# Performance work log

Hardware: AMD Instinct MI355X
Metric: run time of the kernel (lower is better)

## Reference

```python
import jax, jax.numpy as jnp
import numpy as np

NUM_HEADS = 8
NUM_LEVELS = 4
NUM_POINTS = 4


def setup_inputs() -> dict:
    key = jax.random.key(0)
    kq, kp, kv, k1, k2, k3, k4 = jax.random.split(key, 7)
    B, Q, C = 4, 4096, 256
    M, L, P = NUM_HEADS, NUM_LEVELS, NUM_POINTS
    shapes_np = np.array([[128, 128], [64, 64], [32, 32], [16, 16]], dtype=np.int32)
    sizes = shapes_np[:, 0] * shapes_np[:, 1]
    N = int(sizes.sum())  # 21760
    level_index = jnp.asarray(np.concatenate([[0], np.cumsum(sizes)[:-1]]).astype(np.int32))
    q = jax.random.normal(kq, (B, Q, C), jnp.float32)
    p = jax.random.uniform(kp, (B, Q, L, 2), jnp.float32)  # normalized ref points
    v = jax.random.normal(kv, (B, N, C), jnp.float32)
    # proj_offset bias: radial grid init from reset_parameters()
    t = np.arange(M, dtype=np.float32) * (2.0 * np.pi / M)
    grid = np.stack([np.cos(t), np.sin(t)], -1)
    grid = grid / np.abs(grid).max(-1, keepdims=True)
    grid = np.tile(grid[:, None, None, :], (1, L, P, 1)) * np.arange(1, P + 1, dtype=np.float32)[None, None, :, None]
    b_off = jnp.asarray(grid.reshape(-1))
    s = 1.0 / np.sqrt(C).astype(np.float32)
    W_off = jax.random.normal(k1, (C, M * L * P * 2), jnp.float32) * 0.01
    W_attn = jax.random.normal(k2, (C, M * L * P), jnp.float32) * s
    b_attn = jnp.zeros((M * L * P,), jnp.float32)
    W_val = jax.random.normal(k3, (C, C), jnp.float32) * s
    b_val = jnp.zeros((C,), jnp.float32)
    W_out = jax.random.normal(k4, (C, C), jnp.float32) * s
    b_out = jnp.zeros((C,), jnp.float32)
    return {"q": q, "p": p, "v": v, "shapes": jnp.asarray(shapes_np), "level_index": level_index,
            "W_off": W_off, "b_off": b_off, "W_attn": W_attn, "b_attn": b_attn,
            "W_val": W_val, "b_val": b_val, "W_out": W_out, "b_out": b_out}


def _ms_deform_attn(q, p, v, shapes, level_index, W_off, b_off, W_attn, b_attn, W_val, b_val, W_out, b_out):
    B, Q, C = q.shape
    M, L, P = NUM_HEADS, NUM_LEVELS, NUM_POINTS
    D = C // M
    N = v.shape[1]
    # value projection -> [B, M, N, D] (head-major for gather)
    v_p = (v @ W_val + b_val).reshape(B, N, M, D).transpose(0, 2, 1, 3)
    # attention weights, softmax over L*P (classic MSDeformAttn kernel contract)
    attn = jax.nn.softmax((q @ W_attn + b_attn).reshape(B, Q, M, L * P), axis=-1)
    attn = attn.reshape(B, Q, M, L, P)
    # sampling locations (P==2 reference-point branch)
    off = (q @ W_off + b_off).reshape(B, Q, M, L, P, 2)
    norm = jnp.stack([shapes[:, 1], shapes[:, 0]], -1).astype(jnp.float32)  # (W, H) per level
    loc = p[:, :, None, :, None, :] + off / norm[None, None, None, :, None, :]  # [B,Q,M,L,P,2]

    out = jnp.zeros((B, M, Q, D), jnp.float32)
    for l in range(L):
        Hf = shapes[l, 0].astype(jnp.float32)
        Wf = shapes[l, 1].astype(jnp.float32)
        Hi = shapes[l, 0]
        Wi = shapes[l, 1]
        base = level_index[l]
        # grid_sample(align_corners=False) convention: pixel = loc*size - 0.5
        x = loc[:, :, :, l, :, 0] * Wf - 0.5  # [B,Q,M,P]
        y = loc[:, :, :, l, :, 1] * Hf - 0.5
        x0 = jnp.floor(x)
        y0 = jnp.floor(y)
        lx, ly = x - x0, y - y0
        x0i = x0.astype(jnp.int32)
        y0i = y0.astype(jnp.int32)

        def corner(xi, yi, w):
            valid = (xi >= 0) & (xi < Wi) & (yi >= 0) & (yi < Hi)
            idx = base + jnp.clip(yi, 0, Hi - 1) * Wi + jnp.clip(xi, 0, Wi - 1)  # [B,Q,M,P]
            idx = idx.transpose(0, 2, 1, 3).reshape(B, M, Q * P)
            g = jnp.take_along_axis(v_p, idx[..., None], axis=2).reshape(B, M, Q, P, D)
            wv = (w * valid.astype(w.dtype)).transpose(0, 2, 1, 3)[..., None]  # [B,M,Q,P,1]
            return g * wv

        samp = (corner(x0i, y0i, (1 - lx) * (1 - ly))
                + corner(x0i + 1, y0i, lx * (1 - ly))
                + corner(x0i, y0i + 1, (1 - lx) * ly)
                + corner(x0i + 1, y0i + 1, lx * ly))  # [B,M,Q,P,D]
        a_l = attn[:, :, :, l, :].transpose(0, 2, 1, 3)  # [B,M,Q,P]
        out = out + jnp.einsum('bmqpd,bmqp->bmqd', samp, a_l)

    out = out.transpose(0, 2, 1, 3).reshape(B, Q, M * D)
    return out @ W_out + b_out


def reference(q, p, v, shapes, level_index, W_off, b_off, W_attn, b_attn, W_val, b_val, W_out, b_out):
    return _ms_deform_attn(q, p, v, shapes, level_index, W_off, b_off, W_attn, b_attn, W_val, b_val, W_out, b_out)
```

## Files before the change

kernel.cpp:

```cpp
#include <hip/hip_runtime.h>
#include <cstddef>

#define BB 4
#define QQ 4096
#define MM 8
#define NN 21760

typedef __bf16 bf16_8 __attribute__((ext_vector_type(8)));
typedef __bf16 bf16_4 __attribute__((ext_vector_type(4)));
typedef float  floatx4 __attribute__((ext_vector_type(4)));

__global__ __launch_bounds__(256) void prep_weights(
    const float* __restrict__ Wv, const float* __restrict__ Wa,
    const float* __restrict__ Wo, const float* __restrict__ Wu,
    const float* __restrict__ ba, const float* __restrict__ bo,
    __bf16* __restrict__ Wt, float* __restrict__ biasq)
{
    const int gid = blockIdx.x * 256 + threadIdx.x;
    if (gid < 65536) {
        const int n = gid >> 8, k = gid & 255;
        Wt[gid] = (__bf16)Wv[k * 256 + n];
    } else if (gid < 163840) {
        const int o = gid - 65536;
        const int n = o >> 8, k = o & 255;
        Wt[gid] = (__bf16)(n < 128 ? Wa[k * 128 + n] : Wo[k * 256 + (n - 128)]);
    } else if (gid < 229376) {
        const int o = gid - 163840;
        const int n = o >> 8, k = o & 255;
        Wt[gid] = (__bf16)Wu[k * 256 + n];
    } else if (gid < 229760) {
        const int j = gid - 229376;
        biasq[j] = (j < 128) ? ba[j] : bo[j - 128];
    }
}

__global__ __launch_bounds__(512, 4) void gemm_vq(
    const float* __restrict__ v,
    const float* __restrict__ q,
    const __bf16* __restrict__ Wt,
    const float* __restrict__ b_val,
    const float* __restrict__ biasq,
    __bf16* __restrict__ vpb,
    float* __restrict__ gqp)
{
    __shared__ __bf16 As[64][256];

    const int tid  = threadIdx.x;
    const int lane = tid & 63;
    const int wave = tid >> 6;
    const int quad = lane >> 4;
    const int l16  = lane & 15;
    const int flat = blockIdx.x;

    if (flat >= 768) {
        const int f2     = flat - 768;
        const int z      = f2 / 340;
        const int token0 = (f2 - z * 340) * 64;
        const float* Af  = v + (size_t)z * NN * 256;

        #pragma unroll
        for (int c = 0; c < 8; ++c) {
            const int cid = c * 512 + tid;
            const int r   = cid >> 6;
            const int kc  = (cid & 63) * 4;
            const float4 av = *(const float4*)(Af + (size_t)(token0 + r) * 256 + kc);
            bf16_4 w;
            w[0] = (__bf16)av.x; w[1] = (__bf16)av.y;
            w[2] = (__bf16)av.z; w[3] = (__bf16)av.w;
            const int col = ((((kc >> 3) ^ (r & 7)) << 3) | (kc & 7));
            *(bf16_4*)&As[r][col] = w;
        }

        bf16_8 wf[8][2];
        #pragma unroll
        for (int kk = 0; kk < 8; ++kk)
            #pragma unroll
            for (int j = 0; j < 2; ++j)
                wf[kk][j] = *(const bf16_8*)(Wt + (size_t)(wave * 32 + j * 16 + l16) * 256
                                              + kk * 32 + quad * 8);
        __syncthreads();

        floatx4 acc[2][4] = {};
        #pragma unroll
        for (int kk = 0; kk < 8; ++kk) {
            bf16_8 af[4];
            #pragma unroll
            for (int it = 0; it < 4; ++it)
                af[it] = *(const bf16_8*)&As[it * 16 + l16]
                                           [(((kk * 4 + quad) ^ (l16 & 7)) << 3)];
            #pragma unroll
            for (int j = 0; j < 2; ++j)
                #pragma unroll
                for (int it = 0; it < 4; ++it)
                    acc[j][it] = __builtin_amdgcn_mfma_f32_16x16x32_bf16(wf[kk][j], af[it], acc[j][it], 0, 0, 0);
        }

        #pragma unroll
        for (int j = 0; j < 2; ++j) {
            const int n0 = wave * 32 + j * 16 + quad * 4;
            const float4 b4 = *(const float4*)(b_val + n0);
            const int mh = n0 >> 5, dd = n0 & 31;
            #pragma unroll
            for (int it = 0; it < 4; ++it) {
                const int token = token0 + it * 16 + l16;
                bf16_4 ob;
                ob[0] = (__bf16)(acc[j][it][0] + b4.x);
                ob[1] = (__bf16)(acc[j][it][1] + b4.y);
                ob[2] = (__bf16)(acc[j][it][2] + b4.z);
                ob[3] = (__bf16)(acc[j][it][3] + b4.w);
                *(bf16_4*)(vpb + (((size_t)z * 8 + mh) * NN + token) * 32 + dd) = ob;
            }
        }
    } else {
        const int o      = flat;
        const int slice  = o >> 8;
        const int token0 = (o & 255) * 64;
        const int col0   = slice * 128;
        const __bf16* Wb = Wt + 65536 + (size_t)col0 * 256;

        #pragma unroll
        for (int c = 0; c < 8; ++c) {
            const int cid = c * 512 + tid;
            const int r   = cid >> 6;
            const int kc  = (cid & 63) * 4;
            const float4 av = *(const float4*)(q + (size_t)(token0 + r) * 256 + kc);
            bf16_4 w;
            w[0] = (__bf16)av.x; w[1] = (__bf16)av.y;
            w[2] = (__bf16)av.z; w[3] = (__bf16)av.w;
            const int col = ((((kc >> 3) ^ (r & 7)) << 3) | (kc & 7));
            *(bf16_4*)&As[r][col] = w;
        }

        bf16_8 wf[8];
        #pragma unroll
        for (int kk = 0; kk < 8; ++kk)
            wf[kk] = *(const bf16_8*)(Wb + (size_t)(wave * 16 + l16) * 256
                                       + kk * 32 + quad * 8);
        __syncthreads();

        floatx4 acc[4] = {};
        #pragma unroll
        for (int kk = 0; kk < 8; ++kk) {
            bf16_8 af[4];
            #pragma unroll
            for (int it = 0; it < 4; ++it)
                af[it] = *(const bf16_8*)&As[it * 16 + l16]
                                           [(((kk * 4 + quad) ^ (l16 & 7)) << 3)];
            #pragma unroll
            for (int it = 0; it < 4; ++it)
                acc[it] = __builtin_amdgcn_mfma_f32_16x16x32_bf16(wf[kk], af[it], acc[it], 0, 0, 0);
        }

        const int n0 = col0 + wave * 16 + quad * 4;
        const float4 b4 = *(const float4*)(biasq + n0);
        #pragma unroll
        for (int it = 0; it < 4; ++it) {
            const int token = token0 + it * 16 + l16;
            float4 ot;
            ot.x = acc[it][0] + b4.x;
            ot.y = acc[it][1] + b4.y;
            ot.z = acc[it][2] + b4.z;
            ot.w = acc[it][3] + b4.w;
            *(float4*)(gqp + (size_t)token * 384 + n0) = ot;
        }
    }
}

template<typename AT, int NCB, int MODE>
__global__ __launch_bounds__(512, 4) void gemm_ws(
    const AT* __restrict__ A,
    const __bf16* __restrict__ Wn,
    const float* __restrict__ bias,
    void* __restrict__ Cout,
    int tokens, int ldc)
{
    constexpr int F  = NCB / 8;
    constexpr int NJ = F / 16;

    const int z    = blockIdx.z;
    const int col0 = blockIdx.x * NCB;
    const AT* Ab   = A + (size_t)z * tokens * 256;
    const __bf16* Wb = Wn + (size_t)col0 * 256;

    __shared__ __bf16 As[64][256];

    const int tid  = threadIdx.x;
    const int lane = tid & 63;
    const int wave = tid >> 6;
    const int quad = lane >> 4;
    const int l16  = lane & 15;
    const int wave_f = wave * F;

    const int token0 = blockIdx.y * 64;
    if (sizeof(AT) == 4) {
        const float* Af = (const float*)Ab;
        #pragma unroll
        for (int c = 0; c < 8; ++c) {
            const int cid = c * 512 + tid;
            const int r   = cid >> 6;
            const int kc  = (cid & 63) * 4;
            const float4 av = *(const float4*)(Af + (size_t)(token0 + r) * 256 + kc);
            bf16_4 w;
            w[0] = (__bf16)av.x; w[1] = (__bf16)av.y;
            w[2] = (__bf16)av.z; w[3] = (__bf16)av.w;
            const int col = ((((kc >> 3) ^ (r & 7)) << 3) | (kc & 7));
            *(bf16_4*)&As[r][col] = w;
        }
    } else {
        const __bf16* Ah = (const __bf16*)Ab;
        #pragma unroll
        for (int c = 0; c < 4; ++c) {
            const int cid = c * 512 + tid;
            const int r   = cid >> 5;
            const int kc  = (cid & 31) * 8;
            const bf16_8 av = *(const bf16_8*)(Ah + (size_t)(token0 + r) * 256 + kc);
            const int col = (((kc >> 3) ^ (r & 7)) << 3);
            *(bf16_8*)&As[r][col] = av;
        }
    }

    bf16_8 wf[8][NJ];
    #pragma unroll
    for (int kk = 0; kk < 8; ++kk)
        #pragma unroll
        for (int j = 0; j < NJ; ++j)
            wf[kk][j] = *(const bf16_8*)(Wb + (size_t)(wave_f + j * 16 + l16) * 256
                                          + kk * 32 + quad * 8);
    __syncthreads();

    floatx4 acc[NJ][4] = {};
    #pragma unroll
    for (int kk = 0; kk < 8; ++kk) {
        bf16_8 af[4];
        #pragma unroll
        for (int it = 0; it < 4; ++it)
            af[it] = *(const bf16_8*)&As[it * 16 + l16]
                                       [(((kk * 4 + quad) ^ (l16 & 7)) << 3)];
        #pragma unroll
        for (int j = 0; j < NJ; ++j)
            #pragma unroll
            for (int it = 0; it < 4; ++it)
                acc[j][it] = __builtin_amdgcn_mfma_f32_16x16x32_bf16(wf[kk][j], af[it], acc[j][it], 0, 0, 0);
    }

    #pragma unroll
    for (int j = 0; j < NJ; ++j) {
        const int n0 = col0 + wave_f + j * 16 + quad * 4;
        const float4 b4 = *(const float4*)(bias + n0);
        #pragma unroll
        for (int it = 0; it < 4; ++it) {
            const int token = token0 + it * 16 + l16;
            const float v0 = acc[j][it][0] + b4.x;
            const float v1 = acc[j][it][1] + b4.y;
            const float v2 = acc[j][it][2] + b4.z;
            const float v3 = acc[j][it][3] + b4.w;
            if (MODE == 0) {
                float4 o; o.x = v0; o.y = v1; o.z = v2; o.w = v3;
                *(float4*)((float*)Cout + ((size_t)z * tokens + token) * ldc + n0) = o;
            } else {
                const int mh = n0 >> 5, dd = n0 & 31;
                bf16_4 ob;
                ob[0] = (__bf16)v0; ob[1] = (__bf16)v1; ob[2] = (__bf16)v2; ob[3] = (__bf16)v3;
                *(bf16_4*)((__bf16*)Cout + (((size_t)z * 8 + mh) * NN + token) * 32 + dd) = ob;
            }
        }
    }
}

__device__ __forceinline__ float bflo(unsigned u) { return __uint_as_float(u << 16); }
__device__ __forceinline__ float bfhi(unsigned u) { return __uint_as_float(u & 0xffff0000u); }

__global__ __launch_bounds__(512) void sampler(
    const __bf16* __restrict__ vp,
    const float* __restrict__ gqp,
    const float* __restrict__ pref,
    __bf16* __restrict__ mid)
{
    const int t    = threadIdx.x;
    const int m    = t >> 6;
    const int lane = t & 63;
    const int s    = lane >> 2;
    const int c    = lane & 3;
    const int l    = s >> 2;
    const int bq   = blockIdx.x;
    const int b    = bq >> 12;

    const int   Hi = 128 >> l;
    const float Hf = (float)Hi;
    const int   base = (l == 0) ? 0 : (l == 1) ? 16384 : (l == 2) ? 20480 : 21504;

    const float logit = gqp[(size_t)bq * 384 + m * 16 + s];
    const float e = __expf(logit);
    float sum = e;
    #pragma unroll
    for (int k = 4; k < 64; k <<= 1) sum += __shfl_xor(sum, k, 64);
    const float a = e * __builtin_amdgcn_rcpf(sum);

    const float2 off = *(const float2*)(gqp + (size_t)bq * 384 + 128 + (m * 16 + s) * 2);
    const float2 pr  = *(const float2*)(pref + (size_t)bq * 8 + l * 2);

    const float x = fmaf(pr.x, Hf, off.x - 0.5f);
    const float y = fmaf(pr.y, Hf, off.y - 0.5f);
    const float x0f = floorf(x), y0f = floorf(y);
    const float lx = x - x0f, ly = y - y0f;
    const int x0 = (int)x0f, y0 = (int)y0f;
    const int cx0 = min(max(x0, 0), Hi - 1), cx1 = min(max(x0 + 1, 0), Hi - 1);
    const int cy0 = min(max(y0, 0), Hi - 1), cy1 = min(max(y0 + 1, 0), Hi - 1);
    const bool vx0 = (x0 >= 0) && (x0 < Hi), vx1 = (x0 + 1 >= 0) && (x0 + 1 < Hi);
    const bool vy0 = (y0 >= 0) && (y0 < Hi), vy1 = (y0 + 1 >= 0) && (y0 + 1 < Hi);
    const float w00 = a * (1.f - lx) * (1.f - ly) * ((vx0 && vy0) ? 1.f : 0.f);
    const float w10 = a * lx * (1.f - ly) * ((vx1 && vy0) ? 1.f : 0.f);
    const float w01 = a * (1.f - lx) * ly * ((vx0 && vy1) ? 1.f : 0.f);
    const float w11 = a * lx * ly * ((vx1 && vy1) ? 1.f : 0.f);

    const __bf16* vbase = vp + ((size_t)b * 8 + m) * NN * 32;
    const uint4 u00 = *((const uint4*)(vbase + (size_t)(base + cy0 * Hi + cx0) * 32) + c);
    const uint4 u10 = *((const uint4*)(vbase + (size_t)(base + cy0 * Hi + cx1) * 32) + c);
    const uint4 u01 = *((const uint4*)(vbase + (size_t)(base + cy1 * Hi + cx0) * 32) + c);
    const uint4 u11 = *((const uint4*)(vbase + (size_t)(base + cy1 * Hi + cx1) * 32) + c);

    float f[8];
    f[0] = w00*bflo(u00.x) + w10*bflo(u10.x) + w01*bflo(u01.x) + w11*bflo(u11.x);
    f[1] = w00*bfhi(u00.x) + w10*bfhi(u10.x) + w01*bfhi(u01.x) + w11*bfhi(u11.x);
    f[2] = w00*bflo(u00.y) + w10*bflo(u10.y) + w01*bflo(u01.y) + w11*bflo(u11.y);
    f[3] = w00*bfhi(u00.y) + w10*bfhi(u10.y) + w01*bfhi(u01.y) + w11*bfhi(u11.y);
    f[4] = w00*bflo(u00.z) + w10*bflo(u10.z) + w01*bflo(u01.z) + w11*bflo(u11.z);
    f[5] = w00*bfhi(u00.z) + w10*bfhi(u10.z) + w01*bfhi(u01.z) + w11*bfhi(u11.z);
    f[6] = w00*bflo(u00.w) + w10*bflo(u10.w) + w01*bflo(u01.w) + w11*bflo(u11.w);
    f[7] = w00*bfhi(u00.w) + w10*bfhi(u10.w) + w01*bfhi(u01.w) + w11*bfhi(u11.w);

    const int b2 = (lane >> 2) & 1, b3 = (lane >> 3) & 1, b4i = (lane >> 4) & 1;
    #pragma unroll
    for (int j = 0; j < 4; ++j) {
        const float sel  = b2 ? f[j] : f[j + 4];
        const float recv = __shfl_xor(sel, 4, 64);
        f[j] = (b2 ? f[j + 4] : f[j]) + recv;
    }
    #pragma unroll
    for (int j = 0; j < 2; ++j) {
        const float sel  = b3 ? f[j] : f[j + 2];
        const float recv = __shfl_xor(sel, 8, 64);
        f[j] = (b3 ? f[j + 2] : f[j]) + recv;
    }
    {
        const float sel  = b4i ? f[0] : f[1];
        const float recv = __shfl_xor(sel, 16, 64);
        f[0] = (b4i ? f[1] : f[0]) + recv;
    }
    f[0] += __shfl_xor(f[0], 32, 64);

    if (!(lane & 32)) {
        const int chan = (c << 3) | (b2 << 2) | (b3 << 1) | b4i;
        mid[(size_t)bq * 256 + m * 32 + chan] = (__bf16)f[0];
    }
}

extern "C" void kernel_launch(void* const* d_in, const int* in_sizes, int n_in,
                              void* d_out, int out_size, void* d_ws, size_t ws_size,
                              hipStream_t stream) {
    const float* q      = (const float*)d_in[0];
    const float* p      = (const float*)d_in[1];
    const float* v      = (const float*)d_in[2];
    const float* W_off  = (const float*)d_in[5];
    const float* b_off  = (const float*)d_in[6];
    const float* W_attn = (const float*)d_in[7];
    const float* b_attn = (const float*)d_in[8];
    const float* W_val  = (const float*)d_in[9];
    const float* b_val  = (const float*)d_in[10];
    const float* W_out  = (const float*)d_in[11];
    const float* b_out  = (const float*)d_in[12];
    float* out = (float*)d_out;

    float*  gqp   = (float*)d_ws;
    float*  biasq = gqp + (size_t)16384 * 384;
    __bf16* mid   = (__bf16*)(biasq + 384);
    __bf16* vpb   = mid + (size_t)16384 * 256;
    __bf16* Wt    = vpb + (size_t)BB * 8 * NN * 32;
    __bf16* Wt_out = Wt + 163840;

    prep_weights<<<898, 256, 0, stream>>>(W_val, W_attn, W_off, W_out, b_attn, b_off, Wt, biasq);

    gemm_vq<<<2128, 512, 0, stream>>>(v, q, Wt, b_val, biasq, vpb, gqp);

    sampler<<<BB * QQ, 512, 0, stream>>>(vpb, gqp, p, mid);

    {
        dim3 grid(2, 256, 1);
        gemm_ws<__bf16, 128, 0><<<grid, 512, 0, stream>>>(mid, Wt_out, b_out, out, BB * QQ, 256);
    }
}
```

Measured before the change: 246.5 us.

## Fuse bilinear sampler with output projection GEMM via shared-memory tile

Each block now handles 16 queries instead of one. The sampled features go into a swizzled shared-memory tile, and the block then runs the output projection with MFMA directly, so the separate output GEMM kernel and the global 'mid' buffer round trip go away. This removes one launch and the write and re-read of the intermediate. In exchange the sampler work per block is a serial 16-iteration loop, the grid is smaller (1024 blocks), and each block reloads its W_out slice, which may reduce latency hiding for the gathers.

```diff
diff --git a/kernel.cpp b/kernel.cpp
--- a/kernel.cpp
+++ b/kernel.cpp
@@ -166,192 +166,135 @@
     }
 }
 
-template<typename AT, int NCB, int MODE>
-__global__ __launch_bounds__(512, 4) void gemm_ws(
-    const AT* __restrict__ A,
-    const __bf16* __restrict__ Wn,
-    const float* __restrict__ bias,
-    void* __restrict__ Cout,
-    int tokens, int ldc)
-{
-    constexpr int F  = NCB / 8;
-    constexpr int NJ = F / 16;
-
-    const int z    = blockIdx.z;
-    const int col0 = blockIdx.x * NCB;
-    const AT* Ab   = A + (size_t)z * tokens * 256;
-    const __bf16* Wb = Wn + (size_t)col0 * 256;
-
-    __shared__ __bf16 As[64][256];
-
-    const int tid  = threadIdx.x;
-    const int lane = tid & 63;
-    const int wave = tid >> 6;
-    const int quad = lane >> 4;
-    const int l16  = lane & 15;
-    const int wave_f = wave * F;
-
-    const int token0 = blockIdx.y * 64;
-    if (sizeof(AT) == 4) {
-        const float* Af = (const float*)Ab;
-        #pragma unroll
-        for (int c = 0; c < 8; ++c) {
-            const int cid = c * 512 + tid;
-            const int r   = cid >> 6;
-            const int kc  = (cid & 63) * 4;
-            const float4 av = *(const float4*)(Af + (size_t)(token0 + r) * 256 + kc);
-            bf16_4 w;
-            w[0] = (__bf16)av.x; w[1] = (__bf16)av.y;
-            w[2] = (__bf16)av.z; w[3] = (__bf16)av.w;
-            const int col = ((((kc >> 3) ^ (r & 7)) << 3) | (kc & 7));
-            *(bf16_4*)&As[r][col] = w;
-        }
-    } else {
-        const __bf16* Ah = (const __bf16*)Ab;
-        #pragma unroll
-        for (int c = 0; c < 4; ++c) {
-            const int cid = c * 512 + tid;
-            const int r   = cid >> 5;
-            const int kc  = (cid & 31) * 8;
-            const bf16_8 av = *(const bf16_8*)(Ah + (size_t)(token0 + r) * 256 + kc);
-            const int col = (((kc >> 3) ^ (r & 7)) << 3);
-            *(bf16_8*)&As[r][col] = av;
-        }
-    }
-
-    bf16_8 wf[8][NJ];
-    #pragma unroll
-    for (int kk = 0; kk < 8; ++kk)
-        #pragma unroll
-        for (int j = 0; j < NJ; ++j)
-            wf[kk][j] = *(const bf16_8*)(Wb + (size_t)(wave_f + j * 16 + l16) * 256
-                                          + kk * 32 + quad * 8);
-    __syncthreads();
-
-    floatx4 acc[NJ][4] = {};
-    #pragma unroll
-    for (int kk = 0; kk < 8; ++kk) {
-        bf16_8 af[4];
-        #pragma unroll
-        for (int it = 0; it < 4; ++it)
-            af[it] = *(const bf16_8*)&As[it * 16 + l16]
-                                       [(((kk * 4 + quad) ^ (l16 & 7)) << 3)];
-        #pragma unroll
-        for (int j = 0; j < NJ; ++j)
-            #pragma unroll
-            for (int it = 0; it < 4; ++it)
-                acc[j][it] = __builtin_amdgcn_mfma_f32_16x16x32_bf16(wf[kk][j], af[it], acc[j][it], 0, 0, 0);
-    }
-
-    #pragma unroll
-    for (int j = 0; j < NJ; ++j) {
-        const int n0 = col0 + wave_f + j * 16 + quad * 4;
-        const float4 b4 = *(const float4*)(bias + n0);
-        #pragma unroll
-        for (int it = 0; it < 4; ++it) {
-            const int token = token0 + it * 16 + l16;
-            const float v0 = acc[j][it][0] + b4.x;
-            const float v1 = acc[j][it][1] + b4.y;
-            const float v2 = acc[j][it][2] + b4.z;
-            const float v3 = acc[j][it][3] + b4.w;
-            if (MODE == 0) {
-                float4 o; o.x = v0; o.y = v1; o.z = v2; o.w = v3;
-                *(float4*)((float*)Cout + ((size_t)z * tokens + token) * ldc + n0) = o;
-            } else {
-                const int mh = n0 >> 5, dd = n0 & 31;
-                bf16_4 ob;
-                ob[0] = (__bf16)v0; ob[1] = (__bf16)v1; ob[2] = (__bf16)v2; ob[3] = (__bf16)v3;
-                *(bf16_4*)((__bf16*)Cout + (((size_t)z * 8 + mh) * NN + token) * 32 + dd) = ob;
-            }
-        }
-    }
-}
-
 __device__ __forceinline__ float bflo(unsigned u) { return __uint_as_float(u << 16); }
 __device__ __forceinline__ float bfhi(unsigned u) { return __uint_as_float(u & 0xffff0000u); }
 
-__global__ __launch_bounds__(512) void sampler(
+__global__ __launch_bounds__(512) void sampler_out(
     const __bf16* __restrict__ vp,
     const float* __restrict__ gqp,
     const float* __restrict__ pref,
-    __bf16* __restrict__ mid)
+    const __bf16* __restrict__ Wout,
+    const float* __restrict__ b_out,
+    float* __restrict__ out)
 {
+    __shared__ __bf16 mids[16][256];
+
     const int t    = threadIdx.x;
     const int m    = t >> 6;
     const int lane = t & 63;
     const int s    = lane >> 2;
     const int c    = lane & 3;
     const int l    = s >> 2;
-    const int bq   = blockIdx.x;
-    const int b    = bq >> 12;
+    const int bq0  = blockIdx.x * 16;
 
     const int   Hi = 128 >> l;
     const float Hf = (float)Hi;
     const int   base = (l == 0) ? 0 : (l == 1) ? 16384 : (l == 2) ? 20480 : 21504;
-
-    const float logit = gqp[(size_t)bq * 384 + m * 16 + s];
-    const float e = __expf(logit);
-    float sum = e;
+    const int b2 = (lane >> 2) & 1, b3 = (lane >> 3) & 1, b4i = (lane >> 4) & 1;
+
+    for (int qi = 0; qi < 16; ++qi) {
+        const int bq = bq0 + qi;
+        const int b  = bq >> 12;
+
+        const float logit = gqp[(size_t)bq * 384 + m * 16 + s];
+        const float e = __expf(logit);
+        float sum = e;
+        #pragma unroll
+        for (int k = 4; k < 64; k <<= 1) sum += __shfl_xor(sum, k, 64);
+        const float a = e * __builtin_amdgcn_rcpf(sum);
+
+        const float2 off = *(const float2*)(gqp + (size_t)bq * 384 + 128 + (m * 16 + s) * 2);
+        const float2 pr  = *(const float2*)(pref + (size_t)bq * 8 + l * 2);
+
+        const float x = fmaf(pr.x, Hf, off.x - 0.5f);
+        const float y = fmaf(pr.y, Hf, off.y - 0.5f);
+        const float x0f = floorf(x), y0f = floorf(y);
+        const float lx = x - x0f, ly = y - y0f;
+        const int x0 = (int)x0f, y0 = (int)y0f;
+        const int cx0 = min(max(x0, 0), Hi - 1), cx1 = min(max(x0 + 1, 0), Hi - 1);
+        const int cy0 = min(max(y0, 0), Hi - 1), cy1 = min(max(y0 + 1, 0), Hi - 1);
+        const bool vx0 = (x0 >= 0) && (x0 < Hi), vx1 = (x0 + 1 >= 0) && (x0 + 1 < Hi);
+        const bool vy0 = (y0 >= 0) && (y0 < Hi), vy1 = (y0 + 1 >= 0) && (y0 + 1 < Hi);
+        const float w00 = a * (1.f - lx) * (1.f - ly) * ((vx0 && vy0) ? 1.f : 0.f);
+        const float w10 = a * lx * (1.f - ly) * ((vx1 && vy0) ? 1.f : 0.f);
+        const float w01 = a * (1.f - lx) * ly * ((vx0 && vy1) ? 1.f : 0.f);
+        const float w11 = a * lx * ly * ((vx1 && vy1) ? 1.f : 0.f);
+
+        const __bf16* vbase = vp + ((size_t)b * 8 + m) * NN * 32;
+        const uint4 u00 = *((const uint4*)(vbase + (size_t)(base + cy0 * Hi + cx0) * 32) + c);
+        const uint4 u10 = *((const uint4*)(vbase + (size_t)(base + cy0 * Hi + cx1) * 32) + c);
+        const uint4 u01 = *((const uint4*)(vbase + (size_t)(base + cy1 * Hi + cx0) * 32) + c);
+        const uint4 u11 = *((const uint4*)(vbase + (size_t)(base + cy1 * Hi + cx1) * 32) + c);
+
+        float f[8];
+        f[0] = w00*bflo(u00.x) + w10*bflo(u10.x) + w01*bflo(u01.x) + w11*bflo(u11.x);
+        f[1] = w00*bfhi(u00.x) + w10*bfhi(u10.x) + w01*bfhi(u01.x) + w11*bfhi(u11.x);
+        f[2] = w00*bflo(u00.y) + w10*bflo(u10.y) + w01*bflo(u01.y) + w11*bflo(u11.y);
+        f[3] = w00*bfhi(u00.y) + w10*bfhi(u10.y) + w01*bfhi(u01.y) + w11*bfhi(u11.y);
+        f[4] = w00*bflo(u00.z) + w10*bflo(u10.z) + w01*bflo(u01.z) + w11*bflo(u11.z);
+        f[5] = w00*bfhi(u00.z) + w10*bfhi(u10.z) + w01*bfhi(u01.z) + w11*bfhi(u11.z);
+        f[6] = w00*bflo(u00.w) + w10*bflo(u10.w) + w01*bflo(u01.w) + w11*bflo(u11.w);
+        f[7] = w00*bfhi(u00.w) + w10*bfhi(u10.w) + w01*bfhi(u01.w) + w11*bfhi(u11.w);
+
+        #pragma unroll
+        for (int j = 0; j < 4; ++j) {
+            const float sel  = b2 ? f[j] : f[j + 4];
+            const float recv = __shfl_xor(sel, 4, 64);
+            f[j] = (b2 ? f[j + 4] : f[j]) + recv;
+        }
+        #pragma unroll
+        for (int j = 0; j < 2; ++j) {
+            const float sel  = b3 ? f[j] : f[j + 2];
+            const float recv = __shfl_xor(sel, 8, 64);
+            f[j] = (b3 ? f[j + 2] : f[j]) + recv;
+        }
+        {
+            const float sel  = b4i ? f[0] : f[1];
+            const float recv = __shfl_xor(sel, 16, 64);
+            f[0] = (b4i ? f[1] : f[0]) + recv;
+        }
+        f[0] += __shfl_xor(f[0], 32, 64);
+
+        if (!(lane & 32)) {
+            const int chan = (c << 3) | (b2 << 2) | (b3 << 1) | b4i;
+            const int cf   = m * 32 + chan;
+            const int p = ((((cf >> 3) ^ (qi & 7)) << 3) | (cf & 7));
+            mids[qi][p] = (__bf16)f[0];
+        }
+    }
+    __syncthreads();
+
+    const int quad = lane >> 4;
+    const int l16  = lane & 15;
+
+    bf16_8 wf[8][2];
     #pragma unroll
-    for (int k = 4; k < 64; k <<= 1) sum += __shfl_xor(sum, k, 64);
-    const float a = e * __builtin_amdgcn_rcpf(sum);
-
-    const float2 off = *(const float2*)(gqp + (size_t)bq * 384 + 128 + (m * 16 + s) * 2);
-    const float2 pr  = *(const float2*)(pref + (size_t)bq * 8 + l * 2);
-
-    const float x = fmaf(pr.x, Hf, off.x - 0.5f);
-    const float y = fmaf(pr.y, Hf, off.y - 0.5f);
-    const float x0f = floorf(x), y0f = floorf(y);
-    const float lx = x - x0f, ly = y - y0f;
-    const int x0 = (int)x0f, y0 = (int)y0f;
-    const int cx0 = min(max(x0, 0), Hi - 1), cx1 = min(max(x0 + 1, 0), Hi - 1);
-    const int cy0 = min(max(y0, 0), Hi - 1), cy1 = min(max(y0 + 1, 0), Hi - 1);
-    const bool vx0 = (x0 >= 0) && (x0 < Hi), vx1 = (x0 + 1 >= 0) && (x0 + 1 < Hi);
-    const bool vy0 = (y0 >= 0) && (y0 < Hi), vy1 = (y0 + 1 >= 0) && (y0 + 1 < Hi);
-    const float w00 = a * (1.f - lx) * (1.f - ly) * ((vx0 && vy0) ? 1.f : 0.f);
-    const float w10 = a * lx * (1.f - ly) * ((vx1 && vy0) ? 1.f : 0.f);
-    const float w01 = a * (1.f - lx) * ly * ((vx0 && vy1) ? 1.f : 0.f);
-    const float w11 = a * lx * ly * ((vx1 && vy1) ? 1.f : 0.f);
-
-    const __bf16* vbase = vp + ((size_t)b * 8 + m) * NN * 32;
-    const uint4 u00 = *((const uint4*)(vbase + (size_t)(base + cy0 * Hi + cx0) * 32) + c);
-    const uint4 u10 = *((const uint4*)(vbase + (size_t)(base + cy0 * Hi + cx1) * 32) + c);
-    const uint4 u01 = *((const uint4*)(vbase + (size_t)(base + cy1 * Hi + cx0) * 32) + c);
-    const uint4 u11 = *((const uint4*)(vbase + (size_t)(base + cy1 * Hi + cx1) * 32) + c);
-
-    float f[8];
-    f[0] = w00*bflo(u00.x) + w10*bflo(u10.x) + w01*bflo(u01.x) + w11*bflo(u11.x);
-    f[1] = w00*bfhi(u00.x) + w10*bfhi(u10.x) + w01*bfhi(u01.x) + w11*bfhi(u11.x);
-    f[2] = w00*bflo(u00.y) + w10*bflo(u10.y) + w01*bflo(u01.y) + w11*bflo(u11.y);
-    f[3] = w00*bfhi(u00.y) + w10*bfhi(u10.y) + w01*bfhi(u01.y) + w11*bfhi(u11.y);
-    f[4] = w00*bflo(u00.z) + w10*bflo(u10.z) + w01*bflo(u01.z) + w11*bflo(u11.z);
-    f[5] = w00*bfhi(u00.z) + w10*bfhi(u10.z) + w01*bfhi(u01.z) + w11*bfhi(u11.z);
-    f[6] = w00*bflo(u00.w) + w10*bflo(u10.w) + w01*bflo(u01.w) + w11*bflo(u11.w);
-    f[7] = w00*bfhi(u00.w) + w10*bfhi(u10.w) + w01*bfhi(u01.w) + w11*bfhi(u11.w);
-
-    const int b2 = (lane >> 2) & 1, b3 = (lane >> 3) & 1, b4i = (lane >> 4) & 1;
+    for (int kk = 0; kk < 8; ++kk)
+        #pragma unroll
+        for (int j = 0; j < 2; ++j)
+            wf[kk][j] = *(const bf16_8*)(Wout + (size_t)(m * 32 + j * 16 + l16) * 256
+                                          + kk * 32 + quad * 8);
+
+    floatx4 acc[2] = {};
     #pragma unroll
-    for (int j = 0; j < 4; ++j) {
-        const float sel  = b2 ? f[j] : f[j + 4];
-        const float recv = __shfl_xor(sel, 4, 64);
-        f[j] = (b2 ? f[j + 4] : f[j]) + recv;
-    }
+    for (int kk = 0; kk < 8; ++kk) {
+        const bf16_8 af = *(const bf16_8*)&mids[l16][(((kk * 4 + quad) ^ (l16 & 7)) << 3)];
+        #pragma unroll
+        for (int j = 0; j < 2; ++j)
+            acc[j] = __builtin_amdgcn_mfma_f32_16x16x32_bf16(wf[kk][j], af, acc[j], 0, 0, 0);
+    }
+
     #pragma unroll
     for (int j = 0; j < 2; ++j) {
-        const float sel  = b3 ? f[j] : f[j + 2];
-        const float recv = __shfl_xor(sel, 8, 64);
-        f[j] = (b3 ? f[j + 2] : f[j]) + recv;
-    }
-    {
-        const float sel  = b4i ? f[0] : f[1];
-        const float recv = __shfl_xor(sel, 16, 64);
-        f[0] = (b4i ? f[1] : f[0]) + recv;
-    }
-    f[0] += __shfl_xor(f[0], 32, 64);
-
-    if (!(lane & 32)) {
-        const int chan = (c << 3) | (b2 << 2) | (b3 << 1) | b4i;
-        mid[(size_t)bq * 256 + m * 32 + chan] = (__bf16)f[0];
+        const int n0 = m * 32 + j * 16 + quad * 4;
+        const float4 b4 = *(const float4*)(b_out + n0);
+        const int token = bq0 + l16;
+        float4 o;
+        o.x = acc[j][0] + b4.x;
+        o.y = acc[j][1] + b4.y;
+        o.z = acc[j][2] + b4.z;
+        o.w = acc[j][3] + b4.w;
+        *(float4*)(out + (size_t)token * 256 + n0) = o;
     }
 }
 
@@ -382,10 +325,5 @@
 
     gemm_vq<<<2128, 512, 0, stream>>>(v, q, Wt, b_val, biasq, vpb, gqp);
 
-    sampler<<<BB * QQ, 512, 0, stream>>>(vpb, gqp, p, mid);
-
-    {
-        dim3 grid(2, 256, 1);
-        gemm_ws<__bf16, 128, 0><<<grid, 512, 0, stream>>>(mid, Wt_out, b_out, out, BB * QQ, 256);
-    }
+    sampler_out<<<1024, 512, 0, stream>>>(vpb, gqp, p, Wt_out, b_out, out);
 }
```

Measured after the change: 261.9 us. +6.3%, slower.
